# Performance work log

Measured on AMD Instinct MI355X. Metric: run time of the kernel, lower is better.

Reference implementation:

```python
import jax, jax.numpy as jnp
import numpy as np

V, E, H = 50000, 300, 512
T, BIO, BIO_E = 9, 10, 64
REL_E, R = 128, 50
B, L = 16, 128


def _lstm(x, wih, whh, bih, bhh):
    # x: [B, L, E]; PyTorch gate order i, f, g, o
    h0 = jnp.zeros((x.shape[0], whh.shape[1]), x.dtype)
    def step(carry, xt):
        h, c = carry
        g = xt @ wih.T + h @ whh.T + (bih + bhh)
        i, f, gg, o = jnp.split(g, 4, axis=-1)
        c = jax.nn.sigmoid(f) * c + jax.nn.sigmoid(i) * jnp.tanh(gg)
        h = jax.nn.sigmoid(o) * jnp.tanh(c)
        return (h, c), h
    _, hs = jax.lax.scan(step, (h0, h0), jnp.swapaxes(x, 0, 1))
    return jnp.swapaxes(hs, 0, 1)


def _crf_nll(emi, tags, mask, trans, start, end):
    # torchcrf-style linear-chain CRF NLL, mean reduction. emi: [B,L,T]
    mf = mask.astype(emi.dtype)
    ar = jnp.arange(emi.shape[0])
    emi_t = jnp.swapaxes(emi, 0, 1)   # [L,B,T]
    tags_t = jnp.swapaxes(tags, 0, 1)
    mf_t = jnp.swapaxes(mf, 0, 1)
    num0 = start[tags_t[0]] + emi_t[0][ar, tags_t[0]]
    def num_step(carry, inp):
        prev, score = carry
        e_t, t_t, m_t = inp
        score = score + (trans[prev, t_t] + e_t[ar, t_t]) * m_t
        prev = jnp.where(m_t > 0, t_t, prev)
        return (prev, score), None
    (last, num), _ = jax.lax.scan(num_step, (tags_t[0], num0), (emi_t[1:], tags_t[1:], mf_t[1:]))
    num = num + end[last]
    def den_step(alpha, inp):
        e_t, m_t = inp
        nxt = jax.nn.logsumexp(alpha[:, :, None] + trans[None] + e_t[:, None, :], axis=1)
        return jnp.where(m_t[:, None] > 0, nxt, alpha), None
    alpha, _ = jax.lax.scan(den_step, start[None] + emi_t[0], (emi_t[1:], mf_t[1:]))
    den = jax.nn.logsumexp(alpha + end[None], axis=1)
    return -jnp.mean(num - den)


def setup_inputs() -> dict:
    key = jax.random.key(0)
    ks = jax.random.split(key, 24)
    lengths = jax.random.randint(ks[0], (B,), L // 2, L + 1)
    tok = jax.random.randint(ks[1], (B, L), 1, V)
    tokens = jnp.where(jnp.arange(L)[None, :] < lengths[:, None], tok, 0)  # 0 = <pad>
    n = lambda k, shp, s=0.05: jax.random.normal(k, shp, dtype=jnp.float32) * s
    z = lambda shp: jnp.zeros(shp, jnp.float32)
    return dict(
        tokens=tokens,
        bio_gold=jax.random.randint(ks[2], (B, L), 0, T),
        selection_gold=jax.random.randint(ks[3], (B, L, R, L), 0, 2).astype(jnp.int32),
        is_train=1,
        word_emb=n(ks[4], (V, E), 0.02),
        rel_emb=n(ks[5], (R, REL_E), 0.1),
        bio_emb=n(ks[6], (BIO, BIO_E), 0.1),
        w_ih_f=n(ks[7], (4 * H, E)), w_hh_f=n(ks[8], (4 * H, H)),
        b_ih_f=n(ks[9], (4 * H,)), b_hh_f=n(ks[10], (4 * H,)),
        w_ih_b=n(ks[11], (4 * H, E)), w_hh_b=n(ks[12], (4 * H, H)),
        b_ih_b=n(ks[13], (4 * H,)), b_hh_b=n(ks[14], (4 * H,)),
        emission_w=n(ks[15], (T, H)), emission_b=z((T,)),
        sel_u_w=n(ks[16], (REL_E, H + BIO_E)), sel_u_b=z((REL_E,)),
        sel_v_w=n(ks[17], (REL_E, H + BIO_E)), sel_v_b=z((REL_E,)),
        sel_uv_w=n(ks[18], (REL_E, 2 * REL_E)), sel_uv_b=z((REL_E,)),
        crf_trans=n(ks[19], (T, T), 0.1),
        crf_start=n(ks[20], (T,), 0.1),
        crf_end=n(ks[21], (T,), 0.1),
    )


def reference(tokens, bio_gold, selection_gold, is_train, word_emb, rel_emb, bio_emb,
              w_ih_f, w_hh_f, b_ih_f, b_hh_f, w_ih_b, w_hh_b, b_ih_b, b_hh_b,
              emission_w, emission_b, sel_u_w, sel_u_b, sel_v_w, sel_v_b,
              sel_uv_w, sel_uv_b, crf_trans, crf_start, crf_end):
    mask = tokens != 0
    emb = word_emb[tokens]                                 # [B,L,E]
    hf = _lstm(emb, w_ih_f, w_hh_f, b_ih_f, b_hh_f)
    hb = _lstm(emb[:, ::-1], w_ih_b, w_hh_b, b_ih_b, b_hh_b)[:, ::-1]
    o = (hf + hb) * 0.5                                    # avg of the two directions
    emi = o @ emission_w.T + emission_b                    # [B,L,T]
    crf_loss = _crf_nll(emi, bio_gold, mask, crf_trans, crf_start, crf_end)
    oc = jnp.concatenate([o, bio_emb[bio_gold]], axis=-1)  # [B,L,H+BIO_E]
    u = jax.nn.relu(oc @ sel_u_w.T + sel_u_b)              # [B,L,REL_E]
    v = jax.nn.relu(oc @ sel_v_w.T + sel_v_b)
    # linear(concat(u_j, v_i)) == u_j @ W1.T + v_i @ W2.T  (fused, avoids [B,L,L,2R])
    w1, w2 = sel_uv_w[:, :REL_E], sel_uv_w[:, REL_E:]
    uv = jax.nn.relu((u @ w1.T)[:, None, :, :] + (v @ w2.T)[:, :, None, :] + sel_uv_b)  # [B,L,L,REL_E]
    logits = jnp.einsum('bijh,rh->birj', uv, rel_emb)      # [B,L,R,L]
    g = selection_gold.astype(logits.dtype)
    bce = jnp.maximum(logits, 0) - logits * g + jnp.log1p(jnp.exp(-jnp.abs(logits)))
    pm = (mask[:, :, None] & mask[:, None, :])[:, :, None, :].astype(logits.dtype)
    sel_loss = jnp.sum(bce * pm) / jnp.sum(mask).astype(logits.dtype)
    return crf_loss + sel_loss
```

## Files before the change

kernel.cpp:

```cpp
#include <hip/hip_runtime.h>
#include <math.h>

#define NB   16
#define SL   128
#define ED   300
#define HD   512
#define G4   2048
#define NT   9
#define BE   64
#define RE   128
#define NR   50
#define OCD  576
#define NTOK 2048

__device__ __forceinline__ float sigf(float x){ return 1.0f/(1.0f + __expf(-x)); }

template<int TM>
__device__ __forceinline__ void gemm_body(const float* __restrict__ A, int lda,
                                          const float* __restrict__ Bm, int ldb,
                                          float* __restrict__ C, int ldc,
                                          int N, int K,
                                          const float* __restrict__ bias1,
                                          const float* __restrict__ bias2,
                                          int do_relu, int m_blk, int n_blk)
{
    constexpr int TR = TM/16;
    __shared__ float As[16][TM+4];
    __shared__ float Bs[16][68];
    const int t = threadIdx.x;
    const int tm = (t >> 4) * TR;
    const int tn = (t & 15) * 4;
    float acc[TR][4];
    #pragma unroll
    for (int i=0;i<TR;++i){ acc[i][0]=0.f; acc[i][1]=0.f; acc[i][2]=0.f; acc[i][3]=0.f; }

    const int kc = (K + 15) >> 4;
    for (int ck = 0; ck < kc; ++ck){
        const int k0 = ck << 4;
        __syncthreads();
        #pragma unroll
        for (int it = 0; it < TM/64; ++it){
            int task = t + it*256;
            int m = task >> 2, q = task & 3;
            int kk = k0 + q*4;
            float4 v = make_float4(0.f,0.f,0.f,0.f);
            const float* ap = A + (size_t)(m_blk + m)*lda + kk;
            if (kk + 3 < K) v = *(const float4*)ap;
            else {
                if (kk   < K) v.x = ap[0];
                if (kk+1 < K) v.y = ap[1];
                if (kk+2 < K) v.z = ap[2];
            }
            As[q*4+0][m] = v.x; As[q*4+1][m] = v.y; As[q*4+2][m] = v.z; As[q*4+3][m] = v.w;
        }
        {
            int n = t >> 2, q = t & 3;
            int kk = k0 + q*4;
            int gn = n_blk + n;
            float4 v = make_float4(0.f,0.f,0.f,0.f);
            if (gn < N){
                const float* bp = Bm + (size_t)gn*ldb + kk;
                if (kk + 3 < K) v = *(const float4*)bp;
                else {
                    if (kk   < K) v.x = bp[0];
                    if (kk+1 < K) v.y = bp[1];
                    if (kk+2 < K) v.z = bp[2];
                }
            }
            Bs[q*4+0][n] = v.x; Bs[q*4+1][n] = v.y; Bs[q*4+2][n] = v.z; Bs[q*4+3][n] = v.w;
        }
        __syncthreads();
        #pragma unroll
        for (int k = 0; k < 16; ++k){
            float4 b4 = *(const float4*)&Bs[k][tn];
            float bn[4] = {b4.x, b4.y, b4.z, b4.w};
            #pragma unroll
            for (int i = 0; i < TR/4; ++i){
                float4 a4 = *(const float4*)&As[k][tm + i*4];
                float am[4] = {a4.x, a4.y, a4.z, a4.w};
                #pragma unroll
                for (int mm = 0; mm < 4; ++mm){
                    #pragma unroll
                    for (int nn = 0; nn < 4; ++nn)
                        acc[i*4+mm][nn] += am[mm]*bn[nn];
                }
            }
        }
    }
    float bv[4];
    #pragma unroll
    for (int nn=0;nn<4;++nn){
        int gn = n_blk + tn + nn;
        float bb = 0.f;
        if (gn < N){
            if (bias1) bb += bias1[gn];
            if (bias2) bb += bias2[gn];
        }
        bv[nn] = bb;
    }
    bool vec = ((ldc & 3) == 0) && (n_blk + tn + 3 < N);
    #pragma unroll
    for (int mm = 0; mm < TR; ++mm){
        int gm = m_blk + tm + mm;
        float r0 = acc[mm][0] + bv[0];
        float r1 = acc[mm][1] + bv[1];
        float r2 = acc[mm][2] + bv[2];
        float r3 = acc[mm][3] + bv[3];
        if (do_relu){ r0=fmaxf(r0,0.f); r1=fmaxf(r1,0.f); r2=fmaxf(r2,0.f); r3=fmaxf(r3,0.f); }
        if (vec){
            *(float4*)(C + (size_t)gm*ldc + n_blk + tn) = make_float4(r0,r1,r2,r3);
        } else {
            int gn = n_blk + tn;
            if (gn   < N) C[(size_t)gm*ldc + gn  ] = r0;
            if (gn+1 < N) C[(size_t)gm*ldc + gn+1] = r1;
            if (gn+2 < N) C[(size_t)gm*ldc + gn+2] = r2;
            if (gn+3 < N) C[(size_t)gm*ldc + gn+3] = r3;
        }
    }
}

template<int TM>
__global__ __launch_bounds__(256) void gemm_k(const float* __restrict__ A, int lda,
                                              const float* __restrict__ Bm, int ldb,
                                              float* __restrict__ C, int ldc,
                                              int N, int K,
                                              const float* __restrict__ bias1,
                                              const float* __restrict__ bias2,
                                              int do_relu)
{
    gemm_body<TM>(A, lda, Bm, ldb, C, ldc, N, K, bias1, bias2, do_relu,
                  blockIdx.x * TM, blockIdx.y * 64);
}

template<int TM>
__global__ __launch_bounds__(256) void gemm_dual_k(const float* __restrict__ A0, const float* __restrict__ A1, int lda,
                                                   const float* __restrict__ B0, const float* __restrict__ B1, int ldb,
                                                   float* __restrict__ C0, float* __restrict__ C1, int ldc,
                                                   int N, int K,
                                                   const float* __restrict__ bias0, const float* __restrict__ bias1,
                                                   int do_relu)
{
    const int z = blockIdx.z;
    gemm_body<TM>(z ? A1 : A0, lda, z ? B1 : B0, ldb, z ? C1 : C0, ldc, N, K,
                  z ? bias1 : bias0, nullptr, do_relu, blockIdx.x * TM, blockIdx.y * 64);
}

__global__ __launch_bounds__(256) void gather_k(const int* __restrict__ tokens,
                                                const float* __restrict__ word_emb,
                                                float* __restrict__ emb)
{
    int idx = blockIdx.x*256 + threadIdx.x;
    if (idx >= NTOK*75) return;
    int row = idx / 75;
    int c4  = (idx - row*75) * 4;
    const int tok = tokens[row];
    *(float4*)(emb + (size_t)row*ED + c4) = *(const float4*)(word_emb + (size_t)tok*ED + c4);
}

__global__ __launch_bounds__(256) void gemm_xw_k(const float* __restrict__ emb,
                                                 const float* __restrict__ B0, const float* __restrict__ B1,
                                                 float* __restrict__ C0, float* __restrict__ C1,
                                                 const float* __restrict__ bi0a, const float* __restrict__ bi0b,
                                                 const float* __restrict__ bi1a, const float* __restrict__ bi1b)
{
    __shared__ float As[16][132];
    __shared__ float Bs[16][132];
    const int z = blockIdx.z;
    const float* Bm = z ? B1 : B0;
    float* C       = z ? C1 : C0;
    const float* ba = z ? bi1a : bi0a;
    const float* bb = z ? bi1b : bi0b;
    const int t = threadIdx.x;
    const int m_blk = blockIdx.x * 128;
    const int n_blk = blockIdx.y * 128;
    const int tm = (t >> 4) * 8;
    const int tn = (t & 15) * 8;
    float acc[8][8];
    #pragma unroll
    for (int i=0;i<8;++i)
        #pragma unroll
        for (int j=0;j<8;++j) acc[i][j]=0.f;

    for (int ck = 0; ck < 19; ++ck){
        const int k0 = ck << 4;
        __syncthreads();
        #pragma unroll
        for (int it = 0; it < 2; ++it){
            int task = t + it*256;
            int m = task >> 2, q = task & 3;
            int kk = k0 + q*4;
            const float* ap = emb + (size_t)(m_blk + m)*ED + kk;
            float4 v = make_float4(0.f,0.f,0.f,0.f);
            if (kk + 3 < ED) v = *(const float4*)ap;
            else {
                if (kk   < ED) v.x = ap[0];
                if (kk+1 < ED) v.y = ap[1];
                if (kk+2 < ED) v.z = ap[2];
            }
            As[q*4+0][m] = v.x; As[q*4+1][m] = v.y; As[q*4+2][m] = v.z; As[q*4+3][m] = v.w;
        }
        #pragma unroll
        for (int it = 0; it < 2; ++it){
            int task = t + it*256;
            int n = task >> 2, q = task & 3;
            int kk = k0 + q*4;
            const float* bp = Bm + (size_t)(n_blk + n)*ED + kk;
            float4 v = make_float4(0.f,0.f,0.f,0.f);
            if (kk + 3 < ED) v = *(const float4*)bp;
            else {
                if (kk   < ED) v.x = bp[0];
                if (kk+1 < ED) v.y = bp[1];
                if (kk+2 < ED) v.z = bp[2];
            }
            Bs[q*4+0][n] = v.x; Bs[q*4+1][n] = v.y; Bs[q*4+2][n] = v.z; Bs[q*4+3][n] = v.w;
        }
        __syncthreads();
        #pragma unroll
        for (int k = 0; k < 16; ++k){
            float4 b40 = *(const float4*)&Bs[k][tn];
            float4 b41 = *(const float4*)&Bs[k][tn+4];
            float bn[8] = {b40.x,b40.y,b40.z,b40.w,b41.x,b41.y,b41.z,b41.w};
            float4 a40 = *(const float4*)&As[k][tm];
            float4 a41 = *(const float4*)&As[k][tm+4];
            float am[8] = {a40.x,a40.y,a40.z,a40.w,a41.x,a41.y,a41.z,a41.w};
            #pragma unroll
            for (int mm = 0; mm < 8; ++mm){
                #pragma unroll
                for (int nn = 0; nn < 8; ++nn)
                    acc[mm][nn] += am[mm]*bn[nn];
            }
        }
    }
    float bv[8];
    #pragma unroll
    for (int nn=0;nn<8;++nn){ int gn = n_blk + tn + nn; bv[nn] = ba[gn] + bb[gn]; }
    #pragma unroll
    for (int mm = 0; mm < 8; ++mm){
        int gm = m_blk + tm + mm;
        *(float4*)(C + (size_t)gm*G4 + n_blk + tn) =
            make_float4(acc[mm][0]+bv[0], acc[mm][1]+bv[1], acc[mm][2]+bv[2], acc[mm][3]+bv[3]);
        *(float4*)(C + (size_t)gm*G4 + n_blk + tn + 4) =
            make_float4(acc[mm][4]+bv[4], acc[mm][5]+bv[5], acc[mm][6]+bv[6], acc[mm][7]+bv[7]);
    }
}

__device__ __forceinline__ unsigned long long agld(const unsigned long long* p){
    return __hip_atomic_load(p, __ATOMIC_RELAXED, __HIP_MEMORY_SCOPE_AGENT);
}
__device__ __forceinline__ void agst(unsigned long long* p, unsigned long long v){
    __hip_atomic_store(p, v, __ATOMIC_RELAXED, __HIP_MEMORY_SCOPE_AGENT);
}
__device__ __forceinline__ bool tagok(unsigned long long a, unsigned long long b,
                                      unsigned long long c, unsigned long long d, unsigned w){
    return ((unsigned)(a>>32)==w) & ((unsigned)(b>>32)==w) &
           ((unsigned)(c>>32)==w) & ((unsigned)(d>>32)==w);
}

__global__ __launch_bounds__(256, 2) void lstm_k(const float* __restrict__ xwf,
                                                 const float* __restrict__ xwb,
                                                 const float* __restrict__ whhf,
                                                 const float* __restrict__ whhb,
                                                 unsigned long long* __restrict__ hteam,
                                                 float* __restrict__ hf_all,
                                                 float* __restrict__ hb_all)
{
    __shared__ __align__(16) float h_s[2*HD];
    __shared__ __align__(16) float part[8*128];
    __shared__ float gates_s[128];
    __shared__ float cst[32];
    const int wg   = blockIdx.x;
    const int dir  = wg >> 8;
    const int id8  = wg & 255;
    const int team = id8 >> 5;
    const int rank = id8 & 31;
    const int b0   = team * 2;
    const int t    = threadIdx.x;
    const int wv   = t >> 6;
    const int lane = t & 63;
    const int rg   = t & 31;
    const int kc   = t >> 5;
    const int lr0  = rg*2, lr1 = rg*2 + 1;
    const int grow0 = (lr0 >> 4)*HD + rank*16 + (lr0 & 15);
    const int grow1 = (lr1 >> 4)*HD + rank*16 + (lr1 & 15);
    const float* xw   = dir ? xwb    : xwf;
    const float* whh  = dir ? whhb   : whhf;
    float*       hall = dir ? hb_all : hf_all;
    unsigned long long* hT = hteam + (size_t)((team*2 + dir)*2)*1024;

    float4 w0[16], w1[16];
    {
        const float* p0 = whh + (size_t)grow0*HD + kc*64;
        const float* p1 = whh + (size_t)grow1*HD + kc*64;
        #pragma unroll
        for (int q = 0; q < 16; ++q){
            w0[q] = *(const float4*)(p0 + q*4);
            w1[q] = *(const float4*)(p1 + q*4);
        }
    }
    const int rrow = t >> 1, rb2 = t & 1;
    const int growr = (rrow >> 4)*HD + rank*16 + (rrow & 15);
    const int ahl = t >> 1, ab2 = t & 1;
    const int hidx_a = rank*16 + ahl;
    const int s0 = wv*128 + lane;

    if (t < 32) cst[t] = 0.f;
    __syncthreads();

    int par = 0;
    for (int s = 0; s < SL; ++s){
        const unsigned want = (unsigned)s;
        const int sx = dir ? (SL-1 - s) : s;
        float xval = 0.f;
        if (t < 128)
            xval = xw[(size_t)((b0 + rb2)*SL + sx)*G4 + growr];
        {
            const unsigned long long* src = hT + (size_t)par*1024;
            unsigned long long v0, v1, v2, v3;
            for (;;){
                v0 = agld(&src[      s0     ]);
                v1 = agld(&src[      s0 + 64]);
                v2 = agld(&src[512 + s0     ]);
                v3 = agld(&src[512 + s0 + 64]);
                if (tagok(v0,v1,v2,v3,want)) break;
                __builtin_amdgcn_s_sleep(1);
            }
            h_s[     s0     ] = __uint_as_float((unsigned)v0);
            h_s[     s0 + 64] = __uint_as_float((unsigned)v1);
            h_s[HD + s0     ] = __uint_as_float((unsigned)v2);
            h_s[HD + s0 + 64] = __uint_as_float((unsigned)v3);
        }
        {
            float a00=0.f,a01=0.f,a10=0.f,a11=0.f;
            #pragma unroll
            for (int q = 0; q < 16; ++q){
                float4 wa = w0[q], wb = w1[q];
                float4 h0 = *(const float4*)(h_s + 0*HD + kc*64 + q*4);
                float4 h1 = *(const float4*)(h_s + 1*HD + kc*64 + q*4);
                a00 += wa.x*h0.x + wa.y*h0.y + wa.z*h0.z + wa.w*h0.w;
                a01 += wa.x*h1.x + wa.y*h1.y + wa.z*h1.z + wa.w*h1.w;
                a10 += wb.x*h0.x + wb.y*h0.y + wb.z*h0.z + wb.w*h0.w;
                a11 += wb.x*h1.x + wb.y*h1.y + wb.z*h1.z + wb.w*h1.w;
            }
            *(float4*)&part[kc*128 + lr0*2] = make_float4(a00,a01,a10,a11);
        }
        __syncthreads();
        if (t < 128){
            float g = 0.f;
            #pragma unroll
            for (int c = 0; c < 8; ++c) g += part[c*128 + t];
            gates_s[t] = g + xval;
        }
        __syncthreads();
        if (t < 32){
            float gi  = gates_s[(0*16 + ahl)*2 + ab2];
            float gf  = gates_s[(1*16 + ahl)*2 + ab2];
            float gc  = gates_s[(2*16 + ahl)*2 + ab2];
            float go_ = gates_s[(3*16 + ahl)*2 + ab2];
            float cp = cst[t];
            float cn = sigf(gf)*cp + sigf(gi)*tanhf(gc);
            float hn = sigf(go_)*tanhf(cn);
            cst[t] = cn;
            unsigned long long pk = ((unsigned long long)(unsigned)(s+1) << 32)
                                  | (unsigned long long)__float_as_uint(hn);
            agst(&hT[(size_t)(par^1)*1024 + ab2*512 + hidx_a], pk);
            hall[(size_t)((b0 + ab2)*SL + sx)*HD + hidx_a] = hn;
        }
        par ^= 1;
    }
}

__global__ __launch_bounds__(256) void combine_k(const float* __restrict__ hf,
                                                 const float* __restrict__ hb,
                                                 const int* __restrict__ bio_gold,
                                                 const float* __restrict__ bio_emb,
                                                 float* __restrict__ oc)
{
    int idx = blockIdx.x*256 + threadIdx.x;
    if (idx >= NTOK*144) return;
    int row = idx / 144;
    int c4 = (idx - row*144) * 4;
    float4 v;
    if (c4 < HD){
        float4 a = *(const float4*)(hf + (size_t)row*HD + c4);
        float4 b = *(const float4*)(hb + (size_t)row*HD + c4);
        v = make_float4(0.5f*(a.x+b.x), 0.5f*(a.y+b.y), 0.5f*(a.z+b.z), 0.5f*(a.w+b.w));
    } else {
        int bg = bio_gold[row];
        v = *(const float4*)(bio_emb + bg*BE + (c4 - HD));
    }
    *(float4*)(oc + (size_t)row*OCD + c4) = v;
}

__global__ __launch_bounds__(64) void crf_k(const float* __restrict__ emi,
                                            const int* __restrict__ tags,
                                            const int* __restrict__ tokens,
                                            const float* __restrict__ trans,
                                            const float* __restrict__ startv,
                                            const float* __restrict__ endv,
                                            float* __restrict__ out_crf,
                                            float* __restrict__ out_m)
{
    const int b = blockIdx.x, lane = threadIdx.x;
    unsigned long long m0 = __ballot(tokens[b*SL + lane] != 0);
    unsigned long long m1 = __ballot(tokens[b*SL + 64 + lane] != 0);
    const int len = __popcll(m0) + __popcll(m1);
    float npart = 0.f;
    #pragma unroll
    for (int half = 0; half < 2; ++half){
        int tt = lane + half*64;
        if (tt >= 1 && tt < len){
            int tp = tags[b*SL + tt - 1], tc = tags[b*SL + tt];
            npart += trans[tp*NT + tc] + emi[(size_t)(b*SL + tt)*NT + tc];
        }
    }
    #pragma unroll
    for (int off = 32; off > 0; off >>= 1) npart += __shfl_down(npart, off);
    float tr[NT]; float alpha = -1e30f;
    if (lane < NT){
        #pragma unroll
        for (int i = 0; i < NT; ++i) tr[i] = trans[i*NT + lane];
        alpha = startv[lane] + emi[(size_t)(b*SL)*NT + lane];
    }
    for (int tt = 1; tt < SL; ++tt){
        float al[NT];
        #pragma unroll
        for (int i = 0; i < NT; ++i) al[i] = __shfl(alpha, i);
        if (lane < NT && tt < len){
            float mx = -1e30f;
            #pragma unroll
            for (int i = 0; i < NT; ++i) mx = fmaxf(mx, al[i] + tr[i]);
            float se = 0.f;
            #pragma unroll
            for (int i = 0; i < NT; ++i) se += __expf(al[i] + tr[i] - mx);
            alpha = mx + __logf(se) + emi[(size_t)(b*SL + tt)*NT + lane];
        }
    }
    float alf = (lane < NT) ? (alpha + endv[lane]) : -1e30f;
    float alE[NT];
    #pragma unroll
    for (int i = 0; i < NT; ++i) alE[i] = __shfl(alf, i);
    if (lane == 0){
        float mx = -1e30f;
        #pragma unroll
        for (int i = 0; i < NT; ++i) mx = fmaxf(mx, alE[i]);
        float se = 0.f;
        #pragma unroll
        for (int i = 0; i < NT; ++i) se += __expf(alE[i] - mx);
        float den = mx + __logf(se);
        int t0g = tags[b*SL];
        float num = startv[t0g] + emi[(size_t)(b*SL)*NT + t0g] + npart;
        num += endv[tags[b*SL + len - 1]];
        atomicAdd(out_crf, -(num - den) * (1.0f/16.0f));
        atomicAdd(out_m, (float)len);
    }
}

__global__ __launch_bounds__(256) void sel_k(const float* __restrict__ U2,
                                             const float* __restrict__ V2,
                                             const float* __restrict__ uvb,
                                             const float* __restrict__ rel_emb,
                                             const int* __restrict__ gold,
                                             const int* __restrict__ tokens,
                                             float* __restrict__ out_sel)
{
    __shared__ float ret_s[RE][52];
    __shared__ float pt_s[RE][68];
    __shared__ float vb_s[RE];
    __shared__ float mk_s[64];
    __shared__ float red_s[4];
    const int jt = blockIdx.x, qi = blockIdx.y, b = blockIdx.z;
    const int t = threadIdx.x;
    if (tokens[b*SL + qi] == 0) return;
    if (t < 32){
        float4 v4 = *(const float4*)(V2 + (size_t)(b*SL + qi)*RE + t*4);
        float4 b4 = *(const float4*)(uvb + t*4);
        vb_s[t*4+0] = v4.x + b4.x; vb_s[t*4+1] = v4.y + b4.y;
        vb_s[t*4+2] = v4.z + b4.z; vb_s[t*4+3] = v4.w + b4.w;
    }
    if (t < 64) mk_s[t] = (tokens[b*SL + jt*64 + t] != 0) ? 1.f : 0.f;
    {
        int r = t & 63;
        for (int q = t >> 6; q < 32; q += 4){
            if (r < NR){
                float4 e4 = *(const float4*)(rel_emb + (size_t)r*RE + q*4);
                ret_s[q*4+0][r] = e4.x; ret_s[q*4+1][r] = e4.y;
                ret_s[q*4+2][r] = e4.z; ret_s[q*4+3][r] = e4.w;
            } else if (r < 64){
                ret_s[q*4+0][r] = 0.f; ret_s[q*4+1][r] = 0.f;
                ret_s[q*4+2][r] = 0.f; ret_s[q*4+3][r] = 0.f;
            }
        }
    }
    __syncthreads();
    {
        int j = t & 63;
        for (int q = t >> 6; q < 32; q += 4){
            float4 u4 = *(const float4*)(U2 + (size_t)(b*SL + jt*64 + j)*RE + q*4);
            pt_s[q*4+0][j] = fmaxf(u4.x + vb_s[q*4+0], 0.f);
            pt_s[q*4+1][j] = fmaxf(u4.y + vb_s[q*4+1], 0.f);
            pt_s[q*4+2][j] = fmaxf(u4.z + vb_s[q*4+2], 0.f);
            pt_s[q*4+3][j] = fmaxf(u4.w + vb_s[q*4+3], 0.f);
        }
    }
    __syncthreads();
    const int mj = (t & 15) * 4;
    const int nr = (t >> 4) * 4;
    float accv[4][4];
    #pragma unroll
    for (int i=0;i<4;++i){ accv[i][0]=0.f; accv[i][1]=0.f; accv[i][2]=0.f; accv[i][3]=0.f; }
    #pragma unroll 4
    for (int k = 0; k < RE; ++k){
        float4 aj = *(const float4*)&pt_s[k][mj];
        float4 br = *(const float4*)&ret_s[k][nr];
        float am[4] = {aj.x, aj.y, aj.z, aj.w};
        float bn[4] = {br.x, br.y, br.z, br.w};
        #pragma unroll
        for (int mm = 0; mm < 4; ++mm){
            #pragma unroll
            for (int nn = 0; nn < 4; ++nn)
                accv[mm][nn] += am[mm]*bn[nn];
        }
    }
    float lsum = 0.f;
    #pragma unroll
    for (int nn = 0; nn < 4; ++nn){
        int r = nr + nn;
        if (r < NR){
            const int* gp = gold + (size_t)((b*SL + qi)*NR + r)*SL + jt*64 + mj;
            #pragma unroll
            for (int mm = 0; mm < 4; ++mm){
                float l = accv[mm][nn];
                float g = (float)gp[mm];
                float bce = fmaxf(l, 0.f) - l*g + __logf(1.f + __expf(-fabsf(l)));
                lsum += bce * mk_s[mj + mm];
            }
        }
    }
    #pragma unroll
    for (int off = 32; off > 0; off >>= 1) lsum += __shfl_down(lsum, off);
    if ((t & 63) == 0) red_s[t >> 6] = lsum;
    __syncthreads();
    if (t == 0) atomicAdd(out_sel, red_s[0]+red_s[1]+red_s[2]+red_s[3]);
}

__global__ void finalize_k(const float* __restrict__ accum, float* __restrict__ out)
{
    if (threadIdx.x == 0 && blockIdx.x == 0) out[0] = accum[0] + accum[1] / accum[2];
}

extern "C" void kernel_launch(void* const* d_in, const int* in_sizes, int n_in,
                              void* d_out, int out_size, void* d_ws, size_t ws_size,
                              hipStream_t stream)
{
    const int*   tokens    = (const int*)  d_in[0];
    const int*   bio_gold  = (const int*)  d_in[1];
    const int*   sel_gold  = (const int*)  d_in[2];
    const float* word_emb  = (const float*)d_in[4];
    const float* rel_emb   = (const float*)d_in[5];
    const float* bio_emb   = (const float*)d_in[6];
    const float* w_ih_f    = (const float*)d_in[7];
    const float* w_hh_f    = (const float*)d_in[8];
    const float* b_ih_f    = (const float*)d_in[9];
    const float* b_hh_f    = (const float*)d_in[10];
    const float* w_ih_b    = (const float*)d_in[11];
    const float* w_hh_b    = (const float*)d_in[12];
    const float* b_ih_b    = (const float*)d_in[13];
    const float* b_hh_b    = (const float*)d_in[14];
    const float* emission_w= (const float*)d_in[15];
    const float* emission_b= (const float*)d_in[16];
    const float* sel_u_w   = (const float*)d_in[17];
    const float* sel_u_b   = (const float*)d_in[18];
    const float* sel_v_w   = (const float*)d_in[19];
    const float* sel_v_b   = (const float*)d_in[20];
    const float* sel_uv_w  = (const float*)d_in[21];
    const float* sel_uv_b  = (const float*)d_in[22];
    const float* crf_trans = (const float*)d_in[23];
    const float* crf_start = (const float*)d_in[24];
    const float* crf_end   = (const float*)d_in[25];
    (void)in_sizes; (void)n_in; (void)out_size; (void)ws_size;

    float* ws     = (float*)d_ws;
    float* emb    = ws;
    float* xwf    = emb    + (size_t)NTOK*ED;
    float* xwb    = xwf    + (size_t)NTOK*G4;
    float* hf_all = xwb    + (size_t)NTOK*G4;
    float* hb_all = hf_all + (size_t)NTOK*HD;
    float* oc     = hb_all + (size_t)NTOK*HD;
    float* emi    = oc     + (size_t)NTOK*OCD;
    float* u_     = emi    + (size_t)NTOK*NT;
    float* v_     = u_     + (size_t)NTOK*RE;
    float* U2     = v_     + (size_t)NTOK*RE;
    float* V2     = U2     + (size_t)NTOK*RE;
    float* accum  = V2     + (size_t)NTOK*RE;

    unsigned long long* hteam = (unsigned long long*)oc;

    hipMemsetAsync(accum, 0, 4*sizeof(float), stream);
    hipMemsetAsync(hteam, 0, (size_t)8*2*2*1024*sizeof(unsigned long long), stream);

    gather_k<<<(NTOK*75 + 255)/256, 256, 0, stream>>>(tokens, word_emb, emb);
    gemm_xw_k<<<dim3(NTOK/128, G4/128, 2), 256, 0, stream>>>(emb,
                                                             w_ih_f, w_ih_b, xwf, xwb,
                                                             b_ih_f, b_hh_f, b_ih_b, b_hh_b);

    {
        const float *p_xwf = xwf, *p_xwb = xwb, *p_whf = w_hh_f, *p_whb = w_hh_b;
        unsigned long long* p_ht = hteam;
        float *p_hf = hf_all, *p_hb = hb_all;
        void* args[7] = {&p_xwf, &p_xwb, &p_whf, &p_whb, &p_ht, &p_hf, &p_hb};
        hipLaunchCooperativeKernel(lstm_k, dim3(512), dim3(256), args, 0u, stream);
    }

    combine_k<<<(NTOK*144 + 255)/256, 256, 0, stream>>>(hf_all, hb_all, bio_gold, bio_emb, oc);

    gemm_k<64><<<dim3(NTOK/64, 1), 256, 0, stream>>>(oc, OCD, emission_w, HD, emi, NT, NT, HD, emission_b, nullptr, 0);
    gemm_dual_k<64><<<dim3(NTOK/64, 2, 2), 256, 0, stream>>>(oc, oc, OCD, sel_u_w, sel_v_w, OCD,
                                                             u_, v_, RE, RE, OCD, sel_u_b, sel_v_b, 1);
    gemm_dual_k<64><<<dim3(NTOK/64, 2, 2), 256, 0, stream>>>(u_, v_, RE, sel_uv_w, sel_uv_w + RE, 2*RE,
                                                             U2, V2, RE, RE, RE, nullptr, nullptr, 0);

    crf_k<<<NB, 64, 0, stream>>>(emi, bio_gold, tokens, crf_trans, crf_start, crf_end, accum + 0, accum + 2);
    sel_k<<<dim3(2, SL, NB), 256, 0, stream>>>(U2, V2, sel_uv_b, rel_emb, sel_gold, tokens, accum + 1);

    finalize_k<<<1, 1, 0, stream>>>(accum, (float*)d_out);
}
```

Measured before the change: 874.0 us.

## Fuse embedding gather and direction-combine into the consuming GEMM loads

The separate gather kernel is removed: the input-projection GEMM now indexes word_emb through the token ids while loading its A tile. The combine kernel is also removed: the emission and u/v GEMMs build the averaged hidden state plus the BIO embedding on the fly as they load tiles. The two memsets are merged into one by moving the LSTM handoff buffer next to the accumulators. This drops kernel launches and the round trips through the emb and oc intermediates, at the cost of repeated hf/hb reads and extra arithmetic in every GEMM tile load.

```diff
diff --git a/kernel.cpp b/kernel.cpp
--- a/kernel.cpp
+++ b/kernel.cpp
@@ -120,19 +120,6 @@
 }
 
 template<int TM>
-__global__ __launch_bounds__(256) void gemm_k(const float* __restrict__ A, int lda,
-                                              const float* __restrict__ Bm, int ldb,
-                                              float* __restrict__ C, int ldc,
-                                              int N, int K,
-                                              const float* __restrict__ bias1,
-                                              const float* __restrict__ bias2,
-                                              int do_relu)
-{
-    gemm_body<TM>(A, lda, Bm, ldb, C, ldc, N, K, bias1, bias2, do_relu,
-                  blockIdx.x * TM, blockIdx.y * 64);
-}
-
-template<int TM>
 __global__ __launch_bounds__(256) void gemm_dual_k(const float* __restrict__ A0, const float* __restrict__ A1, int lda,
                                                    const float* __restrict__ B0, const float* __restrict__ B1, int ldb,
                                                    float* __restrict__ C0, float* __restrict__ C1, int ldc,
@@ -145,23 +132,134 @@
                   z ? bias1 : bias0, nullptr, do_relu, blockIdx.x * TM, blockIdx.y * 64);
 }
 
-__global__ __launch_bounds__(256) void gather_k(const int* __restrict__ tokens,
-                                                const float* __restrict__ word_emb,
-                                                float* __restrict__ emb)
-{
-    int idx = blockIdx.x*256 + threadIdx.x;
-    if (idx >= NTOK*75) return;
-    int row = idx / 75;
-    int c4  = (idx - row*75) * 4;
-    const int tok = tokens[row];
-    *(float4*)(emb + (size_t)row*ED + c4) = *(const float4*)(word_emb + (size_t)tok*ED + c4);
-}
-
-__global__ __launch_bounds__(256) void gemm_xw_k(const float* __restrict__ emb,
+template<int TM>
+__device__ __forceinline__ void gemm_oc_body(const float* __restrict__ hf,
+                                             const float* __restrict__ hb,
+                                             const int* __restrict__ bio_gold,
+                                             const float* __restrict__ bio_emb,
+                                             const float* __restrict__ Bm, int ldb,
+                                             float* __restrict__ C, int ldc,
+                                             int N, int K,
+                                             const float* __restrict__ bias1,
+                                             int do_relu, int m_blk, int n_blk)
+{
+    constexpr int TR = TM/16;
+    __shared__ float As[16][TM+4];
+    __shared__ float Bs[16][68];
+    const int t = threadIdx.x;
+    const int tm = (t >> 4) * TR;
+    const int tn = (t & 15) * 4;
+    float acc[TR][4];
+    #pragma unroll
+    for (int i=0;i<TR;++i){ acc[i][0]=0.f; acc[i][1]=0.f; acc[i][2]=0.f; acc[i][3]=0.f; }
+
+    const int kc = (K + 15) >> 4;
+    for (int ck = 0; ck < kc; ++ck){
+        const int k0 = ck << 4;
+        __syncthreads();
+        #pragma unroll
+        for (int it = 0; it < TM/64; ++it){
+            int task = t + it*256;
+            int m = task >> 2, q = task & 3;
+            int kk = k0 + q*4;
+            int gm = m_blk + m;
+            float4 v;
+            if (kk < HD){
+                float4 a = *(const float4*)(hf + (size_t)gm*HD + kk);
+                float4 b = *(const float4*)(hb + (size_t)gm*HD + kk);
+                v = make_float4(0.5f*(a.x+b.x), 0.5f*(a.y+b.y), 0.5f*(a.z+b.z), 0.5f*(a.w+b.w));
+            } else {
+                int bg = bio_gold[gm];
+                v = *(const float4*)(bio_emb + (size_t)bg*BE + (kk - HD));
+            }
+            As[q*4+0][m] = v.x; As[q*4+1][m] = v.y; As[q*4+2][m] = v.z; As[q*4+3][m] = v.w;
+        }
+        {
+            int n = t >> 2, q = t & 3;
+            int kk = k0 + q*4;
+            int gn = n_blk + n;
+            float4 v = make_float4(0.f,0.f,0.f,0.f);
+            if (gn < N)
+                v = *(const float4*)(Bm + (size_t)gn*ldb + kk);
+            Bs[q*4+0][n] = v.x; Bs[q*4+1][n] = v.y; Bs[q*4+2][n] = v.z; Bs[q*4+3][n] = v.w;
+        }
+        __syncthreads();
+        #pragma unroll
+        for (int k = 0; k < 16; ++k){
+            float4 b4 = *(const float4*)&Bs[k][tn];
+            float bn[4] = {b4.x, b4.y, b4.z, b4.w};
+            #pragma unroll
+            for (int i = 0; i < TR/4; ++i){
+                float4 a4 = *(const float4*)&As[k][tm + i*4];
+                float am[4] = {a4.x, a4.y, a4.z, a4.w};
+                #pragma unroll
+                for (int mm = 0; mm < 4; ++mm){
+                    #pragma unroll
+                    for (int nn = 0; nn < 4; ++nn)
+                        acc[i*4+mm][nn] += am[mm]*bn[nn];
+                }
+            }
+        }
+    }
+    float bv[4];
+    #pragma unroll
+    for (int nn=0;nn<4;++nn){
+        int gn = n_blk + tn + nn;
+        bv[nn] = (gn < N && bias1) ? bias1[gn] : 0.f;
+    }
+    bool vec = ((ldc & 3) == 0) && (n_blk + tn + 3 < N);
+    #pragma unroll
+    for (int mm = 0; mm < TR; ++mm){
+        int gm = m_blk + tm + mm;
+        float r0 = acc[mm][0] + bv[0];
+        float r1 = acc[mm][1] + bv[1];
+        float r2 = acc[mm][2] + bv[2];
+        float r3 = acc[mm][3] + bv[3];
+        if (do_relu){ r0=fmaxf(r0,0.f); r1=fmaxf(r1,0.f); r2=fmaxf(r2,0.f); r3=fmaxf(r3,0.f); }
+        if (vec){
+            *(float4*)(C + (size_t)gm*ldc + n_blk + tn) = make_float4(r0,r1,r2,r3);
+        } else {
+            int gn = n_blk + tn;
+            if (gn   < N) C[(size_t)gm*ldc + gn  ] = r0;
+            if (gn+1 < N) C[(size_t)gm*ldc + gn+1] = r1;
+            if (gn+2 < N) C[(size_t)gm*ldc + gn+2] = r2;
+            if (gn+3 < N) C[(size_t)gm*ldc + gn+3] = r3;
+        }
+    }
+}
+
+__global__ __launch_bounds__(256) void gemm_emi_k(const float* __restrict__ hf,
+                                                  const float* __restrict__ hb,
+                                                  const int* __restrict__ bio_gold,
+                                                  const float* __restrict__ bio_emb,
+                                                  const float* __restrict__ Bm,
+                                                  float* __restrict__ C,
+                                                  const float* __restrict__ bias)
+{
+    gemm_oc_body<64>(hf, hb, bio_gold, bio_emb, Bm, HD, C, NT, NT, HD, bias, 0,
+                     blockIdx.x * 64, 0);
+}
+
+__global__ __launch_bounds__(256) void gemm_uv_k(const float* __restrict__ hf,
+                                                 const float* __restrict__ hb,
+                                                 const int* __restrict__ bio_gold,
+                                                 const float* __restrict__ bio_emb,
                                                  const float* __restrict__ B0, const float* __restrict__ B1,
                                                  float* __restrict__ C0, float* __restrict__ C1,
-                                                 const float* __restrict__ bi0a, const float* __restrict__ bi0b,
-                                                 const float* __restrict__ bi1a, const float* __restrict__ bi1b)
+                                                 const float* __restrict__ bias0, const float* __restrict__ bias1)
+{
+    const int z = blockIdx.z;
+    gemm_oc_body<64>(hf, hb, bio_gold, bio_emb, z ? B1 : B0, OCD,
+                     z ? C1 : C0, RE, RE, OCD, z ? bias1 : bias0, 1,
+                     blockIdx.x * 64, blockIdx.y * 64);
+}
+
+__global__ __launch_bounds__(256) void gemm_emb_k(const int* __restrict__ tokens,
+                                                  const float* __restrict__ word_emb,
+                                                  const float* __restrict__ B0, const float* __restrict__ B1,
+                                                  float* __restrict__ C0, float* __restrict__ C1,
+                                                  const float* __restrict__ bi0a, const float* __restrict__ bi0b,
+                                                  const float* __restrict__ bi1a, const float* __restrict__ bi1b)
 {
     __shared__ float As[16][132];
     __shared__ float Bs[16][132];
@@ -189,7 +287,8 @@
             int task = t + it*256;
             int m = task >> 2, q = task & 3;
             int kk = k0 + q*4;
-            const float* ap = emb + (size_t)(m_blk + m)*ED + kk;
+            const int tok = tokens[m_blk + m];
+            const float* ap = word_emb + (size_t)tok*ED + kk;
             float4 v = make_float4(0.f,0.f,0.f,0.f);
             if (kk + 3 < ED) v = *(const float4*)ap;
             else {
@@ -367,28 +466,6 @@
         }
         par ^= 1;
     }
-}
-
-__global__ __launch_bounds__(256) void combine_k(const float* __restrict__ hf,
-                                                 const float* __restrict__ hb,
-                                                 const int* __restrict__ bio_gold,
-                                                 const float* __restrict__ bio_emb,
-                                                 float* __restrict__ oc)
-{
-    int idx = blockIdx.x*256 + threadIdx.x;
-    if (idx >= NTOK*144) return;
-    int row = idx / 144;
-    int c4 = (idx - row*144) * 4;
-    float4 v;
-    if (c4 < HD){
-        float4 a = *(const float4*)(hf + (size_t)row*HD + c4);
-        float4 b = *(const float4*)(hb + (size_t)row*HD + c4);
-        v = make_float4(0.5f*(a.x+b.x), 0.5f*(a.y+b.y), 0.5f*(a.z+b.z), 0.5f*(a.w+b.w));
-    } else {
-        int bg = bio_gold[row];
-        v = *(const float4*)(bio_emb + bg*BE + (c4 - HD));
-    }
-    *(float4*)(oc + (size_t)row*OCD + c4) = v;
 }
 
 __global__ __launch_bounds__(64) void crf_k(const float* __restrict__ emi,
@@ -593,15 +670,13 @@
     float* V2     = U2     + (size_t)NTOK*RE;
     float* accum  = V2     + (size_t)NTOK*RE;
 
-    unsigned long long* hteam = (unsigned long long*)oc;
-
-    hipMemsetAsync(accum, 0, 4*sizeof(float), stream);
-    hipMemsetAsync(hteam, 0, (size_t)8*2*2*1024*sizeof(unsigned long long), stream);
-
-    gather_k<<<(NTOK*75 + 255)/256, 256, 0, stream>>>(tokens, word_emb, emb);
-    gemm_xw_k<<<dim3(NTOK/128, G4/128, 2), 256, 0, stream>>>(emb,
-                                                             w_ih_f, w_ih_b, xwf, xwb,
-                                                             b_ih_f, b_hh_f, b_ih_b, b_hh_b);
+    unsigned long long* hteam = (unsigned long long*)(accum + 4);
+
+    hipMemsetAsync(accum, 0, 4*sizeof(float) + (size_t)8*2*2*1024*sizeof(unsigned long long), stream);
+
+    gemm_emb_k<<<dim3(NTOK/128, G4/128, 2), 256, 0, stream>>>(tokens, word_emb,
+                                                              w_ih_f, w_ih_b, xwf, xwb,
+                                                              b_ih_f, b_hh_f, b_ih_b, b_hh_b);
 
     {
         const float *p_xwf = xwf, *p_xwb = xwb, *p_whf = w_hh_f, *p_whb = w_hh_b;
@@ -611,11 +686,11 @@
         hipLaunchCooperativeKernel(lstm_k, dim3(512), dim3(256), args, 0u, stream);
     }
 
-    combine_k<<<(NTOK*144 + 255)/256, 256, 0, stream>>>(hf_all, hb_all, bio_gold, bio_emb, oc);
-
-    gemm_k<64><<<dim3(NTOK/64, 1), 256, 0, stream>>>(oc, OCD, emission_w, HD, emi, NT, NT, HD, emission_b, nullptr, 0);
-    gemm_dual_k<64><<<dim3(NTOK/64, 2, 2), 256, 0, stream>>>(oc, oc, OCD, sel_u_w, sel_v_w, OCD,
-                                                             u_, v_, RE, RE, OCD, sel_u_b, sel_v_b, 1);
+    gemm_emi_k<<<dim3(NTOK/64), 256, 0, stream>>>(hf_all, hb_all, bio_gold, bio_emb,
+                                                  emission_w, emi, emission_b);
+    gemm_uv_k<<<dim3(NTOK/64, 2, 2), 256, 0, stream>>>(hf_all, hb_all, bio_gold, bio_emb,
+                                                       sel_u_w, sel_v_w, u_, v_, sel_u_b, sel_v_b);
+
     gemm_dual_k<64><<<dim3(NTOK/64, 2, 2), 256, 0, stream>>>(u_, v_, RE, sel_uv_w, sel_uv_w + RE, 2*RE,
                                                              U2, V2, RE, RE, RE, nullptr, nullptr, 0);
 
```

New measurement: 921.1 us. +5.4%, slower.
